# Kernel tuning notes

Measured on AMD Instinct MI355X. Metric: run time of the kernel, lower is better.

## Reference

```python
import jax, jax.numpy as jnp
import numpy as np

N = 100000
E = 1600000
IN_C = 128
OUT_C = 32
HEADS = 4
NEG_SLOPE = 0.2


def setup_inputs() -> dict:
    key = jax.random.key(0)
    k1, k2, k3, k4, k5 = jax.random.split(key, 5)
    x = jax.random.normal(k1, (N, IN_C), dtype=jnp.float32)
    edge_index = jax.random.randint(k2, (2, E), 0, N, dtype=jnp.int64)
    # Xavier-ish scaled params
    W = jax.random.normal(k3, (OUT_C * HEADS, IN_C), dtype=jnp.float32) * (1.414 * np.sqrt(2.0 / (IN_C + OUT_C * HEADS)))
    att_l = jax.random.normal(k4, (1, HEADS, OUT_C), dtype=jnp.float32) * 0.1
    att_r = jax.random.normal(k5, (1, HEADS, OUT_C), dtype=jnp.float32) * 0.1
    bias = jnp.zeros((OUT_C * HEADS,), dtype=jnp.float32)
    return {"x": x, "edge_index": edge_index, "W": W, "att_l": att_l, "att_r": att_r, "bias": bias}


def reference(x, edge_index, W, att_l, att_r, bias):
    row, col = edge_index[0], edge_index[1]
    # per-node projection: [N, H, C]
    x_proj = (x @ W.T).reshape(N, HEADS, OUT_C)
    x_i = x_proj[row]          # [E, H, C] gather by source
    x_j = x_proj[col]          # [E, H, C] gather by target
    alpha = (x_i * att_l).sum(-1) + (x_j * att_r).sum(-1)   # [E, H]
    alpha = jnp.where(alpha >= 0, alpha, NEG_SLOPE * alpha)  # leaky_relu
    # edge softmax grouped by row (faithful: plain exp, eps=1e-16)
    alpha_exp = jnp.exp(alpha)
    denom = jax.ops.segment_sum(alpha_exp, row, num_segments=N)  # [N, H]
    alpha = alpha_exp / (denom[row] + 1e-16)
    # weighted scatter-add over all heads at once: [N, H, C]
    out = jax.ops.segment_sum(x_j * alpha[:, :, None], row, num_segments=N)
    out = out.reshape(N, HEADS * OUT_C) + bias
    return out
```

## Files before the change

### kernel.cpp

```cpp
#include <hip/hip_runtime.h>
#include <hip/hip_fp16.h>


constexpr float NEG_SLOPE = 0.2f;
constexpr int TILE_ROWS = 64;
constexpr int SLAB = 2048;
constexpr int EPB = 8192;
constexpr int NB_PAD = 2048;
constexpr int FBMAX = 256;

typedef __attribute__((ext_vector_type(8))) short short8;
typedef __attribute__((ext_vector_type(4))) float f32x4;

__device__ inline short f2bf(float f) {
    unsigned u = __float_as_uint(f);
    return (short)((u + 0x7fffu + ((u >> 16) & 1u)) >> 16);
}

__global__ __launch_bounds__(256) void k_prep(const float* __restrict__ W,
                                              const float* __restrict__ attl,
                                              const float* __restrict__ attr,
                                              short* __restrict__ Wa) {
    int blk = blockIdx.x;
    int t = threadIdx.x;
    if (blk < 64) {
        int i = blk * 256 + t;
        Wa[i] = f2bf(W[i]);
    } else if (blk == 64) {
        for (int s = t; s < 1024; s += 256) {
            int which = s >> 9;
            int h = (s >> 7) & 3;
            int k = s & 127;
            const float* att = which ? attr : attl;
            float acc = 0.f;
#pragma unroll 8
            for (int c = 0; c < 32; ++c)
                acc += att[h * 32 + c] * W[(h * 32 + c) * 128 + k];
            Wa[(128 + which * 4 + h) * 128 + k] = f2bf(acc);
        }
    } else {
        int i = (blk - 65) * 256 + t;
        if (i < 1024) Wa[136 * 128 + i] = 0;
    }
}

__global__ __launch_bounds__(512) void k_fill(const int* __restrict__ ei,
                                              unsigned int* __restrict__ slab,
                                              int* __restrict__ starts,
                                              int E, int NB) {
    __shared__ int s_hist[NB_PAD];
    __shared__ int s_cur[NB_PAD];
    __shared__ unsigned int s_stage[EPB];
    __shared__ int s_wsum[8];

    int fb = blockIdx.x;
    int t = threadIdx.x;
    int lane = t & 63, wv = t >> 6;
    int e0 = fb * EPB;
    int ecnt = min(EPB, E - e0);
    bool full = (ecnt == EPB) && ((E & 3) == 0);

    for (int i = t; i < NB_PAD; i += 512) s_hist[i] = 0;
    __syncthreads();

    const int* rows = ei;
    const int* cols = ei + E;

    if (full) {
        const int4* r4 = (const int4*)rows + (e0 >> 2);
#pragma unroll
        for (int k = 0; k < 4; ++k) {
            int4 ra = r4[k * 512 + t];
            atomicAdd(&s_hist[ra.x >> 6], 1);
            atomicAdd(&s_hist[ra.y >> 6], 1);
            atomicAdd(&s_hist[ra.z >> 6], 1);
            atomicAdd(&s_hist[ra.w >> 6], 1);
        }
    } else {
        for (int j = t; j < ecnt; j += 512)
            atomicAdd(&s_hist[rows[e0 + j] >> 6], 1);
    }
    __syncthreads();

    int b0 = t * 4;
    int c0 = s_hist[b0], c1 = s_hist[b0 + 1], c2 = s_hist[b0 + 2], c3 = s_hist[b0 + 3];
    int p = c0 + c1 + c2 + c3;
    int v = p;
#pragma unroll
    for (int off = 1; off < 64; off <<= 1) {
        int u = __shfl_up(v, off);
        if (lane >= off) v += u;
    }
    if (lane == 63) s_wsum[wv] = v;
    __syncthreads();
    if (t == 0) {
        int run = 0;
#pragma unroll
        for (int w = 0; w < 8; ++w) { int tmp = s_wsum[w]; s_wsum[w] = run; run += tmp; }
    }
    __syncthreads();
    int base = s_wsum[wv] + (v - p);
    int e1 = base + c0, e2 = e1 + c1, e3 = e2 + c2;
    s_hist[b0] = base; s_hist[b0 + 1] = e1; s_hist[b0 + 2] = e2; s_hist[b0 + 3] = e3;
    s_cur[b0] = base;  s_cur[b0 + 1] = e1;  s_cur[b0 + 2] = e2;  s_cur[b0 + 3] = e3;
    size_t sb = (size_t)fb * (NB + 1);
    if (b0 + 0 <= NB) starts[sb + b0 + 0] = base;
    if (b0 + 1 <= NB) starts[sb + b0 + 1] = e1;
    if (b0 + 2 <= NB) starts[sb + b0 + 2] = e2;
    if (b0 + 3 <= NB) starts[sb + b0 + 3] = e3;
    __syncthreads();

    if (full) {
        const int4* r4 = (const int4*)rows + (e0 >> 2);
        const int4* c4 = (const int4*)cols + (e0 >> 2);
#pragma unroll
        for (int k = 0; k < 4; ++k) {
            int4 ra = r4[k * 512 + t];
            int4 ca = c4[k * 512 + t];
            int pos;
            pos = atomicAdd(&s_cur[ra.x >> 6], 1);
            s_stage[pos] = ((unsigned int)ca.x << 6) | (unsigned int)(ra.x & 63);
            pos = atomicAdd(&s_cur[ra.y >> 6], 1);
            s_stage[pos] = ((unsigned int)ca.y << 6) | (unsigned int)(ra.y & 63);
            pos = atomicAdd(&s_cur[ra.z >> 6], 1);
            s_stage[pos] = ((unsigned int)ca.z << 6) | (unsigned int)(ra.z & 63);
            pos = atomicAdd(&s_cur[ra.w >> 6], 1);
            s_stage[pos] = ((unsigned int)ca.w << 6) | (unsigned int)(ra.w & 63);
        }
    } else {
        for (int j = t; j < ecnt; j += 512) {
            int rr = rows[e0 + j], cc = cols[e0 + j];
            int pos = atomicAdd(&s_cur[rr >> 6], 1);
            s_stage[pos] = ((unsigned int)cc << 6) | (unsigned int)(rr & 63);
        }
    }
    __syncthreads();

    uint4* dst = (uint4*)(slab + (size_t)fb * EPB);
    const uint4* src = (const uint4*)s_stage;
    int n4 = (ecnt + 3) >> 2;
    for (int i = t; i < n4; i += 512) dst[i] = src[i];
}

__global__ __launch_bounds__(512) void k_gemm(const float* __restrict__ x,
                                              const short* __restrict__ Wa,
                                              __half* __restrict__ xph,
                                              float* __restrict__ l,
                                              float* __restrict__ r,
                                              int N) {
    __shared__ short s_wa[144 * 136];
    int t = threadIdx.x;
    {
        const short8* g = (const short8*)Wa;
        short8* s = (short8*)s_wa;
        for (int i = t; i < 144 * 16; i += 512) {
            int row = i >> 4, k8 = i & 15;
            s[row * 17 + k8] = g[i];
        }
    }
    __syncthreads();

    int wave = t >> 6, lane = t & 63;
    int li = lane & 15, quad = lane >> 4;
    int base = blockIdx.x * 128 + wave * 16;

    f32x4 acc[9];
#pragma unroll
    for (int nt = 0; nt < 9; ++nt) acc[nt] = (f32x4){0.f, 0.f, 0.f, 0.f};

    int anode = base + li;
    bool avalid = anode < N;
    const float4* x4 = (const float4*)x;
    const short8* wb8 = (const short8*)s_wa;

#pragma unroll
    for (int kc = 0; kc < 4; ++kc) {
        float4 p0 = make_float4(0.f, 0.f, 0.f, 0.f), p1 = p0;
        if (avalid) {
            p0 = x4[(size_t)anode * 32 + kc * 8 + quad * 2];
            p1 = x4[(size_t)anode * 32 + kc * 8 + quad * 2 + 1];
        }
        short8 a;
        a[0] = f2bf(p0.x); a[1] = f2bf(p0.y); a[2] = f2bf(p0.z); a[3] = f2bf(p0.w);
        a[4] = f2bf(p1.x); a[5] = f2bf(p1.y); a[6] = f2bf(p1.z); a[7] = f2bf(p1.w);
#pragma unroll
        for (int nt = 0; nt < 9; ++nt) {
            short8 b = wb8[(nt * 16 + li) * 17 + kc * 4 + quad];
            acc[nt] = __builtin_amdgcn_mfma_f32_16x16x32_bf16(a, b, acc[nt], 0, 0, 0);
        }
    }

#pragma unroll
    for (int j = 0; j < 4; ++j) {
        int node = base + quad * 4 + j;
        if (node >= N) continue;
#pragma unroll
        for (int nt = 0; nt < 8; ++nt)
            xph[(size_t)node * 128 + nt * 16 + li] = __float2half(acc[nt][j]);
        if (li < 4)      l[node * 4 + li] = acc[8][j];
        else if (li < 8) r[node * 4 + li - 4] = acc[8][j];
    }
}

__global__ __launch_bounds__(512) void k_tile(const int* __restrict__ starts,
                                              const unsigned int* __restrict__ slab,
                                              const float* __restrict__ l,
                                              const float* __restrict__ r,
                                              const __half* __restrict__ xph,
                                              const float* __restrict__ bias,
                                              float* __restrict__ out,
                                              int N, int NB, int FB) {
    __shared__ unsigned int s_packed[SLAB];
    __shared__ int s_col[SLAB];
    __shared__ __half s_w[SLAB * 4];
    __shared__ float s_dsum[TILE_ROWS * 4];
    __shared__ float s_l[TILE_ROWS * 4];
    __shared__ int s_start[TILE_ROWS + 1];
    __shared__ int s_cursor[TILE_ROWS];
    __shared__ int s_cnt[TILE_ROWS];
    __shared__ int s_fbase[FBMAX];
    __shared__ int s_foff[FBMAX + 1];
    __shared__ int s_w4[4];

    int b = blockIdx.x;
    int base = b * TILE_ROWS;
    int t = threadIdx.x;
    int lane = t & 63, wv = t >> 6;
    int rows = min(TILE_ROWS, N - base);

    if (t < TILE_ROWS) s_cnt[t] = 0;
    if (t < TILE_ROWS * 4) s_dsum[t] = 0.f;
    if (t < rows * 4) s_l[t] = l[base * 4 + t];

    int myc = 0;
    if (t < FB) {
        const int* sp = starts + (size_t)t * (NB + 1) + b;
        int a0 = sp[0], a1 = sp[1];
        s_fbase[t] = a0;
        myc = a1 - a0;
    }
    int v = 0;
    if (t < 256) {
        v = myc;
#pragma unroll
        for (int off = 1; off < 64; off <<= 1) {
            int u = __shfl_up(v, off);
            if (lane >= off) v += u;
        }
        if (lane == 63) s_w4[wv] = v;
    }
    __syncthreads();
    if (t == 0) {
        int run = 0;
#pragma unroll
        for (int w = 0; w < 4; ++w) { int tmp = s_w4[w]; s_w4[w] = run; run += tmp; }
        s_foff[0] = 0;
    }
    __syncthreads();
    if (t < 256) s_foff[t + 1] = v + s_w4[wv];
    __syncthreads();
    int tot = s_foff[FB];
    if (tot > SLAB) tot = SLAB;

    for (int i = t; i < tot; i += 512) {
        int lo = 0, hi = FB;
        while (hi - lo > 1) {
            int mid = (lo + hi) >> 1;
            if (s_foff[mid] <= i) lo = mid; else hi = mid;
        }
        unsigned int p = slab[(size_t)lo * EPB + s_fbase[lo] + (i - s_foff[lo])];
        s_packed[i] = p;
        atomicAdd(&s_cnt[p & 63], 1);
    }
    __syncthreads();

    if (t < 64) {
        int c = s_cnt[t];
        int vv = c;
#pragma unroll
        for (int off = 1; off < 64; off <<= 1) {
            int u = __shfl_up(vv, off);
            if (t >= off) vv += u;
        }
        s_start[t + 1] = vv;
        if (t == 0) s_start[0] = 0;
        s_cursor[t] = vv - c;
    }
    __syncthreads();

    for (int i = t; i < tot; i += 512) {
        unsigned int p = s_packed[i];
        int row = (int)(p & 63);
        int col = (int)(p >> 6);
        int pos = atomicAdd(&s_cursor[row], 1);
        s_col[pos] = col;
        float4 rv = ((const float4*)r)[col];
        float4 lv = ((const float4*)s_l)[row];
        float w0 = lv.x + rv.x, w1 = lv.y + rv.y;
        float w2 = lv.z + rv.z, w3 = lv.w + rv.w;
        w0 = w0 >= 0.f ? w0 : NEG_SLOPE * w0;
        w1 = w1 >= 0.f ? w1 : NEG_SLOPE * w1;
        w2 = w2 >= 0.f ? w2 : NEG_SLOPE * w2;
        w3 = w3 >= 0.f ? w3 : NEG_SLOPE * w3;
        w0 = __expf(w0); w1 = __expf(w1); w2 = __expf(w2); w3 = __expf(w3);
        ((__half2*)s_w)[pos * 2]     = __floats2half2_rn(w0, w1);
        ((__half2*)s_w)[pos * 2 + 1] = __floats2half2_rn(w2, w3);
        atomicAdd(&s_dsum[row * 4 + 0], w0);
        atomicAdd(&s_dsum[row * 4 + 1], w1);
        atomicAdd(&s_dsum[row * 4 + 2], w2);
        atomicAdd(&s_dsum[row * 4 + 3], w3);
    }
    __syncthreads();

    int quarter = lane >> 4;
    int li = lane & 15;
    int h = li >> 2;
    const float4* xp4g = (const float4*)xph;

    float4 b0 = ((const float4*)bias)[2 * li];
    float4 b1 = ((const float4*)bias)[2 * li + 1];

    for (int rl = wv; rl < rows; rl += 8) {
        int s0 = s_start[rl], s1 = s_start[rl + 1];
        float a0 = 0.f, a1 = 0.f, a2 = 0.f, a3 = 0.f;
        float a4 = 0.f, a5 = 0.f, a6 = 0.f, a7 = 0.f;
        for (int i = s0 + quarter; i < s1; i += 8) {
            int iB = i + 4;
            bool hB = iB < s1;
            int colA = s_col[i];
            float wA = __half2float(s_w[i * 4 + h]);
            int colB = hB ? s_col[iB] : colA;
            float wB = hB ? __half2float(s_w[iB * 4 + h]) : 0.f;
            float4 rawA = xp4g[(size_t)colA * 16 + li];
            float4 rawB = xp4g[(size_t)colB * 16 + li];
            {
                __half2* hp = (__half2*)&rawA;
                float2 f0 = __half22float2(hp[0]);
                float2 f1 = __half22float2(hp[1]);
                float2 f2 = __half22float2(hp[2]);
                float2 f3 = __half22float2(hp[3]);
                a0 += wA * f0.x; a1 += wA * f0.y;
                a2 += wA * f1.x; a3 += wA * f1.y;
                a4 += wA * f2.x; a5 += wA * f2.y;
                a6 += wA * f3.x; a7 += wA * f3.y;
            }
            {
                __half2* hp = (__half2*)&rawB;
                float2 f0 = __half22float2(hp[0]);
                float2 f1 = __half22float2(hp[1]);
                float2 f2 = __half22float2(hp[2]);
                float2 f3 = __half22float2(hp[3]);
                a0 += wB * f0.x; a1 += wB * f0.y;
                a2 += wB * f1.x; a3 += wB * f1.y;
                a4 += wB * f2.x; a5 += wB * f2.y;
                a6 += wB * f3.x; a7 += wB * f3.y;
            }
        }
        a0 += __shfl_xor(a0, 16); a0 += __shfl_xor(a0, 32);
        a1 += __shfl_xor(a1, 16); a1 += __shfl_xor(a1, 32);
        a2 += __shfl_xor(a2, 16); a2 += __shfl_xor(a2, 32);
        a3 += __shfl_xor(a3, 16); a3 += __shfl_xor(a3, 32);
        a4 += __shfl_xor(a4, 16); a4 += __shfl_xor(a4, 32);
        a5 += __shfl_xor(a5, 16); a5 += __shfl_xor(a5, 32);
        a6 += __shfl_xor(a6, 16); a6 += __shfl_xor(a6, 32);
        a7 += __shfl_xor(a7, 16); a7 += __shfl_xor(a7, 32);
        if (quarter == 0) {
            float inv = 1.f / (s_dsum[rl * 4 + h] + 1e-16f);
            float4 o0, o1;
            o0.x = a0 * inv + b0.x; o0.y = a1 * inv + b0.y;
            o0.z = a2 * inv + b0.z; o0.w = a3 * inv + b0.w;
            o1.x = a4 * inv + b1.x; o1.y = a5 * inv + b1.y;
            o1.z = a6 * inv + b1.z; o1.w = a7 * inv + b1.w;
            ((float4*)out)[(size_t)(base + rl) * 32 + 2 * li] = o0;
            ((float4*)out)[(size_t)(base + rl) * 32 + 2 * li + 1] = o1;
        }
    }
}

extern "C" void kernel_launch(void* const* d_in, const int* in_sizes, int n_in,
                              void* d_out, int out_size, void* d_ws, size_t ws_size,
                              hipStream_t stream) {
    const float* x    = (const float*)d_in[0];
    const int*   ei   = (const int*)d_in[1];
    const float* W    = (const float*)d_in[2];
    const float* attl = (const float*)d_in[3];
    const float* attr = (const float*)d_in[4];
    const float* bias = (const float*)d_in[5];
    int N = in_sizes[0] / 128;
    int E = in_sizes[1] / 2;
    int NB = (N + TILE_ROWS - 1) / TILE_ROWS;
    int FB = (E + EPB - 1) / EPB;

    char* ws = (char*)d_ws;
    __half* xph = (__half*)ws;   ws += (size_t)N * 128 * 2;
    float* l    = (float*)ws;    ws += (size_t)N * 4 * 4;
    float* r    = (float*)ws;    ws += (size_t)N * 4 * 4;
    short* Wa   = (short*)ws;    ws += 144 * 128 * 2;
    int* starts = (int*)ws;      ws += (size_t)FB * (NB + 1) * 4;
    unsigned int* slab = (unsigned int*)ws; ws += (size_t)FB * EPB * 4;

    float* out = (float*)d_out;
    int GB = (N + 127) / 128;

    k_prep<<<69, 256, 0, stream>>>(W, attl, attr, Wa);
    k_fill<<<FB, 512, 0, stream>>>(ei, slab, starts, E, NB);
    k_gemm<<<GB, 512, 0, stream>>>(x, Wa, xph, l, r, N);
    k_tile<<<NB, 512, 0, stream>>>(starts, slab, l, r, xph, bias, out, N, NB, FB);
}
```

Baseline: 224.6 us.

## Merge fill and GEMM kernels, stage xph stores, recompute softmax denominators

The edge-bucketing fill kernel and the projection GEMM are merged into one launch, with blocks split by index so both independent jobs run concurrently in a shared 48KB LDS buffer. The GEMM output is staged through LDS so half-precision rows are written to global memory as coalesced 16-byte stores. In the tile kernel, the four gathers of r per thread are issued up front so their latency overlaps. The per-row softmax denominators are summed per row and head from the stored half weights, replacing float LDS atomics. Risks are higher LDS pressure for the GEMM blocks, fewer resident blocks, and a denominator that now sums fp16-rounded weights.

New measurement: 204.5 us. -9.0%, faster.

```diff
diff --git a/kernel.cpp b/kernel.cpp
--- a/kernel.cpp
+++ b/kernel.cpp
@@ -44,112 +44,114 @@
     }
 }
 
-__global__ __launch_bounds__(512) void k_fill(const int* __restrict__ ei,
-                                              unsigned int* __restrict__ slab,
-                                              int* __restrict__ starts,
-                                              int E, int NB) {
-    __shared__ int s_hist[NB_PAD];
-    __shared__ int s_cur[NB_PAD];
-    __shared__ unsigned int s_stage[EPB];
+__global__ __launch_bounds__(512) void k_fg(const float* __restrict__ x,
+                                            const short* __restrict__ Wa,
+                                            const int* __restrict__ ei,
+                                            __half* __restrict__ xph,
+                                            float* __restrict__ l,
+                                            float* __restrict__ r,
+                                            unsigned int* __restrict__ slab,
+                                            int* __restrict__ starts,
+                                            int N, int E, int NB, int FB) {
+    __shared__ __align__(16) char smem[49152];
     __shared__ int s_wsum[8];
-
-    int fb = blockIdx.x;
     int t = threadIdx.x;
     int lane = t & 63, wv = t >> 6;
-    int e0 = fb * EPB;
-    int ecnt = min(EPB, E - e0);
-    bool full = (ecnt == EPB) && ((E & 3) == 0);
-
-    for (int i = t; i < NB_PAD; i += 512) s_hist[i] = 0;
-    __syncthreads();
-
-    const int* rows = ei;
-    const int* cols = ei + E;
-
-    if (full) {
-        const int4* r4 = (const int4*)rows + (e0 >> 2);
-#pragma unroll
-        for (int k = 0; k < 4; ++k) {
-            int4 ra = r4[k * 512 + t];
-            atomicAdd(&s_hist[ra.x >> 6], 1);
-            atomicAdd(&s_hist[ra.y >> 6], 1);
-            atomicAdd(&s_hist[ra.z >> 6], 1);
-            atomicAdd(&s_hist[ra.w >> 6], 1);
-        }
-    } else {
-        for (int j = t; j < ecnt; j += 512)
-            atomicAdd(&s_hist[rows[e0 + j] >> 6], 1);
-    }
-    __syncthreads();
-
-    int b0 = t * 4;
-    int c0 = s_hist[b0], c1 = s_hist[b0 + 1], c2 = s_hist[b0 + 2], c3 = s_hist[b0 + 3];
-    int p = c0 + c1 + c2 + c3;
-    int v = p;
-#pragma unroll
-    for (int off = 1; off < 64; off <<= 1) {
-        int u = __shfl_up(v, off);
-        if (lane >= off) v += u;
-    }
-    if (lane == 63) s_wsum[wv] = v;
-    __syncthreads();
-    if (t == 0) {
-        int run = 0;
-#pragma unroll
-        for (int w = 0; w < 8; ++w) { int tmp = s_wsum[w]; s_wsum[w] = run; run += tmp; }
-    }
-    __syncthreads();
-    int base = s_wsum[wv] + (v - p);
-    int e1 = base + c0, e2 = e1 + c1, e3 = e2 + c2;
-    s_hist[b0] = base; s_hist[b0 + 1] = e1; s_hist[b0 + 2] = e2; s_hist[b0 + 3] = e3;
-    s_cur[b0] = base;  s_cur[b0 + 1] = e1;  s_cur[b0 + 2] = e2;  s_cur[b0 + 3] = e3;
-    size_t sb = (size_t)fb * (NB + 1);
-    if (b0 + 0 <= NB) starts[sb + b0 + 0] = base;
-    if (b0 + 1 <= NB) starts[sb + b0 + 1] = e1;
-    if (b0 + 2 <= NB) starts[sb + b0 + 2] = e2;
-    if (b0 + 3 <= NB) starts[sb + b0 + 3] = e3;
-    __syncthreads();
-
-    if (full) {
-        const int4* r4 = (const int4*)rows + (e0 >> 2);
-        const int4* c4 = (const int4*)cols + (e0 >> 2);
-#pragma unroll
-        for (int k = 0; k < 4; ++k) {
-            int4 ra = r4[k * 512 + t];
-            int4 ca = c4[k * 512 + t];
-            int pos;
-            pos = atomicAdd(&s_cur[ra.x >> 6], 1);
-            s_stage[pos] = ((unsigned int)ca.x << 6) | (unsigned int)(ra.x & 63);
-            pos = atomicAdd(&s_cur[ra.y >> 6], 1);
-            s_stage[pos] = ((unsigned int)ca.y << 6) | (unsigned int)(ra.y & 63);
-            pos = atomicAdd(&s_cur[ra.z >> 6], 1);
-            s_stage[pos] = ((unsigned int)ca.z << 6) | (unsigned int)(ra.z & 63);
-            pos = atomicAdd(&s_cur[ra.w >> 6], 1);
-            s_stage[pos] = ((unsigned int)ca.w << 6) | (unsigned int)(ra.w & 63);
-        }
-    } else {
-        for (int j = t; j < ecnt; j += 512) {
-            int rr = rows[e0 + j], cc = cols[e0 + j];
-            int pos = atomicAdd(&s_cur[rr >> 6], 1);
-            s_stage[pos] = ((unsigned int)cc << 6) | (unsigned int)(rr & 63);
-        }
-    }
-    __syncthreads();
-
-    uint4* dst = (uint4*)(slab + (size_t)fb * EPB);
-    const uint4* src = (const uint4*)s_stage;
-    int n4 = (ecnt + 3) >> 2;
-    for (int i = t; i < n4; i += 512) dst[i] = src[i];
-}
-
-__global__ __launch_bounds__(512) void k_gemm(const float* __restrict__ x,
-                                              const short* __restrict__ Wa,
-                                              __half* __restrict__ xph,
-                                              float* __restrict__ l,
-                                              float* __restrict__ r,
-                                              int N) {
-    __shared__ short s_wa[144 * 136];
-    int t = threadIdx.x;
+
+    if ((int)blockIdx.x < FB) {
+        int* s_hist = (int*)smem;
+        int* s_cur  = (int*)(smem + 8192);
+        unsigned int* s_stage = (unsigned int*)(smem + 16384);
+
+        int fb = blockIdx.x;
+        int e0 = fb * EPB;
+        int ecnt = min(EPB, E - e0);
+        bool full = (ecnt == EPB) && ((E & 3) == 0);
+
+        for (int i = t; i < NB_PAD; i += 512) s_hist[i] = 0;
+        __syncthreads();
+
+        const int* rows = ei;
+        const int* cols = ei + E;
+
+        if (full) {
+            const int4* r4 = (const int4*)rows + (e0 >> 2);
+#pragma unroll
+            for (int k = 0; k < 4; ++k) {
+                int4 ra = r4[k * 512 + t];
+                atomicAdd(&s_hist[ra.x >> 6], 1);
+                atomicAdd(&s_hist[ra.y >> 6], 1);
+                atomicAdd(&s_hist[ra.z >> 6], 1);
+                atomicAdd(&s_hist[ra.w >> 6], 1);
+            }
+        } else {
+            for (int j = t; j < ecnt; j += 512)
+                atomicAdd(&s_hist[rows[e0 + j] >> 6], 1);
+        }
+        __syncthreads();
+
+        int b0 = t * 4;
+        int c0 = s_hist[b0], c1 = s_hist[b0 + 1], c2 = s_hist[b0 + 2], c3 = s_hist[b0 + 3];
+        int p = c0 + c1 + c2 + c3;
+        int v = p;
+#pragma unroll
+        for (int off = 1; off < 64; off <<= 1) {
+            int u = __shfl_up(v, off);
+            if (lane >= off) v += u;
+        }
+        if (lane == 63) s_wsum[wv] = v;
+        __syncthreads();
+        if (t == 0) {
+            int run = 0;
+#pragma unroll
+            for (int w = 0; w < 8; ++w) { int tmp = s_wsum[w]; s_wsum[w] = run; run += tmp; }
+        }
+        __syncthreads();
+        int base = s_wsum[wv] + (v - p);
+        int e1 = base + c0, e2 = e1 + c1, e3 = e2 + c2;
+        s_hist[b0] = base; s_hist[b0 + 1] = e1; s_hist[b0 + 2] = e2; s_hist[b0 + 3] = e3;
+        s_cur[b0] = base;  s_cur[b0 + 1] = e1;  s_cur[b0 + 2] = e2;  s_cur[b0 + 3] = e3;
+        size_t sb = (size_t)fb * (NB + 1);
+        if (b0 + 0 <= NB) starts[sb + b0 + 0] = base;
+        if (b0 + 1 <= NB) starts[sb + b0 + 1] = e1;
+        if (b0 + 2 <= NB) starts[sb + b0 + 2] = e2;
+        if (b0 + 3 <= NB) starts[sb + b0 + 3] = e3;
+        __syncthreads();
+
+        if (full) {
+            const int4* r4 = (const int4*)rows + (e0 >> 2);
+            const int4* c4 = (const int4*)cols + (e0 >> 2);
+#pragma unroll
+            for (int k = 0; k < 4; ++k) {
+                int4 ra = r4[k * 512 + t];
+                int4 ca = c4[k * 512 + t];
+                int pos;
+                pos = atomicAdd(&s_cur[ra.x >> 6], 1);
+                s_stage[pos] = ((unsigned int)ca.x << 6) | (unsigned int)(ra.x & 63);
+                pos = atomicAdd(&s_cur[ra.y >> 6], 1);
+                s_stage[pos] = ((unsigned int)ca.y << 6) | (unsigned int)(ra.y & 63);
+                pos = atomicAdd(&s_cur[ra.z >> 6], 1);
+                s_stage[pos] = ((unsigned int)ca.z << 6) | (unsigned int)(ra.z & 63);
+                pos = atomicAdd(&s_cur[ra.w >> 6], 1);
+                s_stage[pos] = ((unsigned int)ca.w << 6) | (unsigned int)(ra.w & 63);
+            }
+        } else {
+            for (int j = t; j < ecnt; j += 512) {
+                int rr = rows[e0 + j], cc = cols[e0 + j];
+                int pos = atomicAdd(&s_cur[rr >> 6], 1);
+                s_stage[pos] = ((unsigned int)cc << 6) | (unsigned int)(rr & 63);
+            }
+        }
+        __syncthreads();
+
+        uint4* dst = (uint4*)(slab + (size_t)fb * EPB);
+        const uint4* src = (const uint4*)s_stage;
+        int n4 = (ecnt + 3) >> 2;
+        for (int i = t; i < n4; i += 512) dst[i] = src[i];
+        return;
+    }
+
+    short* s_wa = (short*)smem;
     {
         const short8* g = (const short8*)Wa;
         short8* s = (short8*)s_wa;
@@ -160,9 +162,9 @@
     }
     __syncthreads();
 
-    int wave = t >> 6, lane = t & 63;
     int li = lane & 15, quad = lane >> 4;
-    int base = blockIdx.x * 128 + wave * 16;
+    int gb = blockIdx.x - FB;
+    int base = gb * 128 + wv * 16;
 
     f32x4 acc[9];
 #pragma unroll
@@ -194,11 +196,30 @@
     for (int j = 0; j < 4; ++j) {
         int node = base + quad * 4 + j;
         if (node >= N) continue;
-#pragma unroll
-        for (int nt = 0; nt < 8; ++nt)
-            xph[(size_t)node * 128 + nt * 16 + li] = __float2half(acc[nt][j]);
         if (li < 4)      l[node * 4 + li] = acc[8][j];
         else if (li < 8) r[node * 4 + li - 4] = acc[8][j];
+    }
+
+    __syncthreads();
+    __half* s_out = (__half*)s_wa;
+#pragma unroll
+    for (int j = 0; j < 4; ++j) {
+        int nl = wv * 16 + quad * 4 + j;
+#pragma unroll
+        for (int nt = 0; nt < 8; ++nt)
+            s_out[nl * 136 + nt * 16 + li] = __float2half(acc[nt][j]);
+    }
+    __syncthreads();
+    {
+        int nl = t >> 2, seg = t & 3;
+        int node = gb * 128 + nl;
+        if (node < N) {
+            const short8* sr = (const short8*)s_wa;
+            short8* xp8 = (short8*)xph;
+#pragma unroll
+            for (int q = 0; q < 4; ++q)
+                xp8[(size_t)node * 16 + seg * 4 + q] = sr[nl * 17 + seg * 4 + q];
+        }
     }
 }
 
@@ -229,7 +250,6 @@
     int rows = min(TILE_ROWS, N - base);
 
     if (t < TILE_ROWS) s_cnt[t] = 0;
-    if (t < TILE_ROWS * 4) s_dsum[t] = 0.f;
     if (t < rows * 4) s_l[t] = l[base * 4 + t];
 
     int myc = 0;
@@ -288,27 +308,52 @@
     }
     __syncthreads();
 
-    for (int i = t; i < tot; i += 512) {
-        unsigned int p = s_packed[i];
-        int row = (int)(p & 63);
-        int col = (int)(p >> 6);
-        int pos = atomicAdd(&s_cursor[row], 1);
-        s_col[pos] = col;
-        float4 rv = ((const float4*)r)[col];
-        float4 lv = ((const float4*)s_l)[row];
-        float w0 = lv.x + rv.x, w1 = lv.y + rv.y;
-        float w2 = lv.z + rv.z, w3 = lv.w + rv.w;
-        w0 = w0 >= 0.f ? w0 : NEG_SLOPE * w0;
-        w1 = w1 >= 0.f ? w1 : NEG_SLOPE * w1;
-        w2 = w2 >= 0.f ? w2 : NEG_SLOPE * w2;
-        w3 = w3 >= 0.f ? w3 : NEG_SLOPE * w3;
-        w0 = __expf(w0); w1 = __expf(w1); w2 = __expf(w2); w3 = __expf(w3);
-        ((__half2*)s_w)[pos * 2]     = __floats2half2_rn(w0, w1);
-        ((__half2*)s_w)[pos * 2 + 1] = __floats2half2_rn(w2, w3);
-        atomicAdd(&s_dsum[row * 4 + 0], w0);
-        atomicAdd(&s_dsum[row * 4 + 1], w1);
-        atomicAdd(&s_dsum[row * 4 + 2], w2);
-        atomicAdd(&s_dsum[row * 4 + 3], w3);
+    {
+        int row_[4], col_[4];
+        bool val_[4];
+#pragma unroll
+        for (int s = 0; s < 4; ++s) {
+            int i = t + s * 512;
+            bool valid = i < tot;
+            unsigned int p = valid ? s_packed[i] : 0u;
+            row_[s] = (int)(p & 63);
+            col_[s] = valid ? (int)(p >> 6) : 0;
+            val_[s] = valid;
+        }
+        float4 rv0 = ((const float4*)r)[col_[0]];
+        float4 rv1 = ((const float4*)r)[col_[1]];
+        float4 rv2 = ((const float4*)r)[col_[2]];
+        float4 rv3 = ((const float4*)r)[col_[3]];
+#pragma unroll
+        for (int s = 0; s < 4; ++s) {
+            if (!val_[s]) continue;
+            float4 rv = s == 0 ? rv0 : s == 1 ? rv1 : s == 2 ? rv2 : rv3;
+            int row = row_[s];
+            int pos = atomicAdd(&s_cursor[row], 1);
+            s_col[pos] = col_[s];
+            float4 lv = ((const float4*)s_l)[row];
+            float w0 = lv.x + rv.x, w1 = lv.y + rv.y;
+            float w2 = lv.z + rv.z, w3 = lv.w + rv.w;
+            w0 = w0 >= 0.f ? w0 : NEG_SLOPE * w0;
+            w1 = w1 >= 0.f ? w1 : NEG_SLOPE * w1;
+            w2 = w2 >= 0.f ? w2 : NEG_SLOPE * w2;
+            w3 = w3 >= 0.f ? w3 : NEG_SLOPE * w3;
+            w0 = __expf(w0); w1 = __expf(w1); w2 = __expf(w2); w3 = __expf(w3);
+            ((__half2*)s_w)[pos * 2]     = __floats2half2_rn(w0, w1);
+            ((__half2*)s_w)[pos * 2 + 1] = __floats2half2_rn(w2, w3);
+        }
+    }
+    __syncthreads();
+
+    if (t < 256) {
+        int row = t >> 2, h = t & 3;
+        if (row < rows) {
+            int s0 = s_start[row], s1 = s_start[row + 1];
+            float d = 0.f;
+            for (int i = s0; i < s1; ++i)
+                d += __half2float(s_w[i * 4 + h]);
+            s_dsum[t] = d;
+        }
     }
     __syncthreads();
 
@@ -403,7 +448,6 @@
     int GB = (N + 127) / 128;
 
     k_prep<<<69, 256, 0, stream>>>(W, attl, attr, Wa);
-    k_fill<<<FB, 512, 0, stream>>>(ei, slab, starts, E, NB);
-    k_gemm<<<GB, 512, 0, stream>>>(x, Wa, xph, l, r, N);
+    k_fg<<<FB + GB, 512, 0, stream>>>(x, Wa, ei, xph, l, r, slab, starts, N, E, NB, FB);
     k_tile<<<NB, 512, 0, stream>>>(starts, slab, l, r, xph, bias, out, N, NB, FB);
 }
```
